# Kernel tuning notes

Hardware: AMD Instinct MI355X
Metric: run time of the kernel (lower is better)

Reference implementation:

```python
import jax, jax.numpy as jnp
import numpy as np

B, D, H, NSTEPS = 4096, 512, 2048, 16


def setup_inputs() -> dict:
    key = jax.random.key(0)
    k1, k2, k3, k4 = jax.random.split(key, 4)
    s_x = 1.0 / np.sqrt(D)
    s_h = 1.0 / np.sqrt(H)
    return {
        "z_in": jax.random.normal(k1, (B, D), dtype=jnp.float32),
        "Wx": jax.random.normal(k2, (D, H), dtype=jnp.float32) * s_x,
        "Wh": jax.random.normal(k3, (H, H), dtype=jnp.float32) * s_h,
        "bh": jnp.zeros((H,), dtype=jnp.float32),
        "Wout": jax.random.normal(k4, (H, D), dtype=jnp.float32) * s_h,
        "bout": jnp.zeros((D,), dtype=jnp.float32),
        "n_steps": NSTEPS,
    }


def reference(z_in, Wx, Wh, bh, Wout, bout, n_steps):
    # Input projection is identical every step (same z_in fed each iteration).
    xproj = z_in @ Wx + bh  # [B, H]
    h0 = jnp.zeros((z_in.shape[0], Wh.shape[0]), dtype=z_in.dtype)

    def step(h, _):
        h_new = jnp.tanh(xproj + h @ Wh)          # Elman RNN cell, hidden retained
        out = h_new @ Wout + bout                  # MLP head hidden -> latent
        return h_new, out

    _, outs = jax.lax.scan(step, h0, None, length=n_steps)  # [n_steps, B, D]
    return jnp.transpose(outs, (1, 0, 2))  # torch.stack(outs, 1) -> [B, n_steps, D]
```

## Files before the change

### kernel.cpp

```cpp
#include <hip/hip_runtime.h>
#include <hip/hip_bf16.h>
#include <stdint.h>

#define B_ 4096
#define D_ 512
#define H_ 2048
#define NS_ 16

typedef __bf16 bf16x8 __attribute__((ext_vector_type(8)));
typedef float f32x4 __attribute__((ext_vector_type(4)));
typedef short short4v __attribute__((ext_vector_type(4)));

__device__ __forceinline__ short f2bf(float f) {
  union { float f; uint32_t u; } c; c.f = f;
  uint32_t u = c.u;
  return (short)((u + 0x7fffu + ((u >> 16) & 1u)) >> 16);
}

__device__ __forceinline__ float tanh_fast(float x) {
  float e = __expf(2.0f * x);
  return 1.0f - 2.0f / (e + 1.0f);
}

__device__ __forceinline__ void gload16(const void* g, void* l) {
  __builtin_amdgcn_global_load_lds((const __attribute__((address_space(1))) void*)g,
                                   (__attribute__((address_space(3))) void*)l,
                                   16, 0, 0);
}

template<int BM, int BN, int EPI>
__global__ __launch_bounds__(256, 2) void gemm_bt(
    const short* __restrict__ A, const short* __restrict__ Bt, int K,
    const float* __restrict__ xproj, const float* __restrict__ bias,
    float* __restrict__ outf, short* __restrict__ outh, int ldN, int tout)
{
  constexpr int WM = BM / 2, WN = BN / 2;
  constexpr int RM = WM / 16, RN = WN / 16;
  __shared__ short lds[2][(BM + BN) * 32];
  const int tid = threadIdx.x, lane = tid & 63, wid = tid >> 6;
  const int wm = wid >> 1, wn = wid & 1;
  const int row0 = blockIdx.y * BM, col0 = blockIdx.x * BN;
  const short* Ag = A + (size_t)row0 * K;
  const short* Bg = Bt + (size_t)col0 * K;

  f32x4 acc[RM][RN];
#pragma unroll
  for (int m = 0; m < RM; ++m)
#pragma unroll
    for (int n = 0; n < RN; ++n)
      acc[m][n] = (f32x4){0.f, 0.f, 0.f, 0.f};

  const int nt = K >> 5;

  auto stage = [&](int kt, int buf) {
    const short* ga = Ag + (kt << 5);
#pragma unroll
    for (int i = 0; i < BM * 4; i += 256) {
      int slot = i + tid;
      gload16(ga + (size_t)(slot >> 2) * K + ((slot & 3) << 3), &lds[buf][slot * 8]);
    }
    const short* gb = Bg + (kt << 5);
#pragma unroll
    for (int i = 0; i < BN * 4; i += 256) {
      int slot = i + tid;
      gload16(gb + (size_t)(slot >> 2) * K + ((slot & 3) << 3),
              &lds[buf][BM * 32 + slot * 8]);
    }
  };

  stage(0, 0);
  __syncthreads();
  int cur = 0;
  const int kq = (lane >> 4) << 3;
  const int rr = lane & 15;
  for (int kt = 0; kt < nt; ++kt) {
    if (kt + 1 < nt) stage(kt + 1, cur ^ 1);
    const short* la = &lds[cur][(wm * WM) * 32];
    const short* lb = &lds[cur][BM * 32 + (wn * WN) * 32];
    bf16x8 a[RM], b[RN];
#pragma unroll
    for (int m = 0; m < RM; ++m)
      a[m] = *(const bf16x8*)(la + (m * 16 + rr) * 32 + kq);
#pragma unroll
    for (int n = 0; n < RN; ++n)
      b[n] = *(const bf16x8*)(lb + (n * 16 + rr) * 32 + kq);
#pragma unroll
    for (int m = 0; m < RM; ++m)
#pragma unroll
      for (int n = 0; n < RN; ++n)
        acc[m][n] = __builtin_amdgcn_mfma_f32_16x16x32_bf16(a[m], b[n], acc[m][n], 0, 0, 0);
    __syncthreads();
    cur ^= 1;
  }

  const int rb = row0 + wm * WM + ((lane >> 4) << 2);
  const int cb = col0 + wn * WN + (lane & 15);
#pragma unroll
  for (int m = 0; m < RM; ++m) {
#pragma unroll
    for (int n = 0; n < RN; ++n) {
      const int col = cb + n * 16;
#pragma unroll
      for (int r = 0; r < 4; ++r) {
        const int row = rb + m * 16 + r;
        float v = acc[m][n][r];
        if (EPI == 0) {
          outf[(size_t)row * ldN + col] = v + bias[col];
        } else if (EPI == 2) {
          outf[(size_t)row * (NS_ * D_) + tout * D_ + col] = v + bias[col];
        } else {
          if (col < H_) {
            float x = xproj[(size_t)row * H_ + col];
            outh[(size_t)row * H_ + col] = f2bf(tanh_fast(x + v));
          } else {
            int oc = col - H_;
            outf[(size_t)row * (NS_ * D_) + tout * D_ + oc] = v + bias[oc];
          }
        }
      }
    }
  }
}

__global__ void transpose_cvt(const float* __restrict__ in, short* __restrict__ out,
                              int R, int C) {
  __shared__ float tile[32][33];
  const int tx = threadIdx.x & 31, ty = threadIdx.x >> 5;
  const int c0 = blockIdx.x * 32, r0 = blockIdx.y * 32;
#pragma unroll
  for (int i = 0; i < 32; i += 8)
    tile[ty + i][tx] = in[(size_t)(r0 + ty + i) * C + c0 + tx];
  __syncthreads();
#pragma unroll
  for (int i = 0; i < 32; i += 8)
    out[(size_t)(c0 + ty + i) * R + r0 + tx] = f2bf(tile[tx][ty + i]);
}

__global__ void cvt_bf16_k(const float4* __restrict__ in, short4v* __restrict__ out, int n4) {
  int i = blockIdx.x * 256 + threadIdx.x;
  if (i >= n4) return;
  float4 v = in[i];
  short4v o;
  o[0] = f2bf(v.x); o[1] = f2bf(v.y); o[2] = f2bf(v.z); o[3] = f2bf(v.w);
  out[i] = o;
}

__global__ void tanh_h0_k(const float4* __restrict__ xp, short4v* __restrict__ h, int n4) {
  int i = blockIdx.x * 256 + threadIdx.x;
  if (i >= n4) return;
  float4 v = xp[i];
  short4v o;
  o[0] = f2bf(tanh_fast(v.x)); o[1] = f2bf(tanh_fast(v.y));
  o[2] = f2bf(tanh_fast(v.z)); o[3] = f2bf(tanh_fast(v.w));
  h[i] = o;
}

extern "C" void kernel_launch(void* const* d_in, const int* in_sizes, int n_in,
                              void* d_out, int out_size, void* d_ws, size_t ws_size,
                              hipStream_t stream) {
  const float* z    = (const float*)d_in[0];
  const float* Wx   = (const float*)d_in[1];
  const float* Wh   = (const float*)d_in[2];
  const float* bh   = (const float*)d_in[3];
  const float* Wout = (const float*)d_in[4];
  const float* bout = (const float*)d_in[5];
  float* out = (float*)d_out;

  short* zb    = (short*)d_ws;
  short* WxT   = zb + (size_t)B_ * D_;
  short* WcatT = WxT + (size_t)H_ * D_;
  short* WoutT = WcatT + (size_t)H_ * H_;
  short* h0    = WcatT + (size_t)(H_ + D_) * H_;
  short* h1    = h0 + (size_t)B_ * H_;
  float* xproj = (float*)(h1 + (size_t)B_ * H_);

  cvt_bf16_k<<<(B_ * D_ / 4 + 255) / 256, 256, 0, stream>>>((const float4*)z, (short4v*)zb, B_ * D_ / 4);
  transpose_cvt<<<dim3(H_ / 32, D_ / 32), 256, 0, stream>>>(Wx, WxT, D_, H_);
  transpose_cvt<<<dim3(H_ / 32, H_ / 32), 256, 0, stream>>>(Wh, WcatT, H_, H_);
  transpose_cvt<<<dim3(D_ / 32, H_ / 32), 256, 0, stream>>>(Wout, WoutT, H_, D_);

  gemm_bt<128, 128, 0><<<dim3(H_ / 128, B_ / 128), 256, 0, stream>>>(
      zb, WxT, D_, nullptr, bh, xproj, nullptr, H_, 0);
  tanh_h0_k<<<(B_ * H_ / 4 + 255) / 256, 256, 0, stream>>>((const float4*)xproj, (short4v*)h0, B_ * H_ / 4);

  short* hb[2] = {h0, h1};
  for (int t = 1; t <= 15; ++t) {
    const short* hp = hb[(t - 1) & 1];
    short* hn = hb[t & 1];
    gemm_bt<128, 128, 1><<<dim3((H_ + D_) / 128, B_ / 128), 256, 0, stream>>>(
        hp, WcatT, H_, xproj, bout, out, hn, 0, t - 1);
  }
  gemm_bt<128, 64, 2><<<dim3(D_ / 64, B_ / 128), 256, 0, stream>>>(
      hb[1], WoutT, H_, nullptr, bout, out, nullptr, 0, 15);
}
```

Measured before the change: 1.176 ms.

## Replace recurrent step GEMM with 256x256 tiled, 4-stage pipelined fused kernel

Adds a new kernel for the 15 recurrent steps. It uses 256x256 output tiles with 8 waves, a 4-deep LDS ring buffer fed by direct global-to-LDS loads, and an XOR-swizzled LDS layout to avoid bank conflicts. Explicit vmcnt waits, setprio and sched barriers interleave loads with MFMA, and block indices are remapped in a chiplet-aware way. The goal is higher arithmetic intensity and better latency hiding than the 128x128 double-buffered kernel, at the cost of a 128KB LDS footprint, heavy register pressure and only 160 workgroups.

After: 1.424 ms. +21.1%, slower.

```diff
diff --git a/kernel.cpp b/kernel.cpp
--- a/kernel.cpp
+++ b/kernel.cpp
@@ -26,6 +26,134 @@
   __builtin_amdgcn_global_load_lds((const __attribute__((address_space(1))) void*)g,
                                    (__attribute__((address_space(3))) void*)l,
                                    16, 0, 0);
+}
+
+__global__ __launch_bounds__(512, 2) void gemm256_fused(
+    const short* __restrict__ A, const short* __restrict__ Bt, int K,
+    const float* __restrict__ xproj, const float* __restrict__ bias,
+    float* __restrict__ outf, short* __restrict__ outh, int tout, int gridN)
+{
+  __shared__ short lds[65536];
+  char* const lbase = (char*)lds;
+  const int tid = threadIdx.x, lane = tid & 63, wid = tid >> 6;
+  const int wm = wid >> 2, wn = wid & 3;
+
+  const int nwg = gridDim.x;
+  const int cpx = nwg >> 3;
+  const int swz = ((int)blockIdx.x & 7) * cpx + ((int)blockIdx.x >> 3);
+  const int tm = swz / gridN, tn = swz % gridN;
+  const int row0 = tm * 256, col0 = tn * 256;
+
+  const int NT = K >> 5;
+
+  const int rA0 = wid * 32 + (lane >> 2);
+  const int rA1 = rA0 + 16;
+  const int sl = lane & 3;
+  const short* gA0 = A  + (size_t)(row0 + rA0) * K + ((sl ^ ((rA0 >> 1) & 3)) << 3);
+  const short* gA1 = A  + (size_t)(row0 + rA1) * K + ((sl ^ ((rA1 >> 1) & 3)) << 3);
+  const short* gB0 = Bt + (size_t)(col0 + rA0) * K + ((sl ^ ((rA0 >> 1) & 3)) << 3);
+  const short* gB1 = Bt + (size_t)(col0 + rA1) * K + ((sl ^ ((rA1 >> 1) & 3)) << 3);
+
+  const int rr = lane & 15, s = lane >> 4;
+  int offA[8], offB[4];
+#pragma unroll
+  for (int m = 0; m < 8; ++m) {
+    int r = wm * 128 + m * 16 + rr;
+    offA[m] = r * 64 + ((s ^ ((r >> 1) & 3)) << 4);
+  }
+#pragma unroll
+  for (int n = 0; n < 4; ++n) {
+    int r = wn * 64 + n * 16 + rr;
+    offB[n] = 16384 + r * 64 + ((s ^ ((r >> 1) & 3)) << 4);
+  }
+
+  f32x4 acc[8][4];
+#pragma unroll
+  for (int m = 0; m < 8; ++m)
+#pragma unroll
+    for (int n = 0; n < 4; ++n)
+      acc[m][n] = (f32x4){0.f, 0.f, 0.f, 0.f};
+
+  auto stageA = [&](int kt) {
+    char* da = lbase + (kt & 3) * 32768 + wid * 2048;
+    gload16(gA0 + (size_t)kt * 32, da);
+    gload16(gA1 + (size_t)kt * 32, da + 1024);
+  };
+  auto stageB = [&](int kt) {
+    char* db = lbase + (kt & 3) * 32768 + 16384 + wid * 2048;
+    gload16(gB0 + (size_t)kt * 32, db);
+    gload16(gB1 + (size_t)kt * 32, db + 1024);
+  };
+
+  stageA(0); stageB(0);
+  stageA(1); stageB(1);
+  stageA(2); stageB(2);
+
+  auto tile = [&](int kt, bool issue) {
+    __builtin_amdgcn_sched_barrier(0);
+    __builtin_amdgcn_s_barrier();
+    __builtin_amdgcn_sched_barrier(0);
+    const char* lb = lbase + (kt & 3) * 32768;
+    if (issue) stageA(kt + 3);
+    bf16x8 a[4], b[4];
+#pragma unroll
+    for (int m = 0; m < 4; ++m) a[m] = *(const bf16x8*)(lb + offA[m]);
+#pragma unroll
+    for (int n = 0; n < 4; ++n) b[n] = *(const bf16x8*)(lb + offB[n]);
+    __builtin_amdgcn_s_setprio(1);
+#pragma unroll
+    for (int m = 0; m < 4; ++m)
+#pragma unroll
+      for (int n = 0; n < 4; ++n)
+        acc[m][n] = __builtin_amdgcn_mfma_f32_16x16x32_bf16(a[m], b[n], acc[m][n], 0, 0, 0);
+    __builtin_amdgcn_s_setprio(0);
+    __builtin_amdgcn_sched_barrier(0);
+    if (issue) stageB(kt + 3);
+#pragma unroll
+    for (int m = 0; m < 4; ++m) a[m] = *(const bf16x8*)(lb + offA[4 + m]);
+    __builtin_amdgcn_s_setprio(1);
+#pragma unroll
+    for (int m = 0; m < 4; ++m)
+#pragma unroll
+      for (int n = 0; n < 4; ++n)
+        acc[4 + m][n] = __builtin_amdgcn_mfma_f32_16x16x32_bf16(a[m], b[n], acc[4 + m][n], 0, 0, 0);
+    __builtin_amdgcn_s_setprio(0);
+    __builtin_amdgcn_sched_barrier(0);
+  };
+
+  int kt = 0;
+  for (; kt < NT - 3; ++kt) {
+    asm volatile("s_waitcnt vmcnt(8)" ::: "memory");
+    tile(kt, true);
+  }
+  asm volatile("s_waitcnt vmcnt(8)" ::: "memory");
+  tile(NT - 3, false);
+  asm volatile("s_waitcnt vmcnt(4)" ::: "memory");
+  tile(NT - 2, false);
+  asm volatile("s_waitcnt vmcnt(0)" ::: "memory");
+  tile(NT - 1, false);
+
+  const int rb = row0 + wm * 128 + ((lane >> 4) << 2);
+  const int cb = col0 + wn * 64 + (lane & 15);
+#pragma unroll
+  for (int m = 0; m < 8; ++m) {
+#pragma unroll
+    for (int n = 0; n < 4; ++n) {
+      const int col = cb + n * 16;
+#pragma unroll
+      for (int r = 0; r < 4; ++r) {
+        const int row = rb + m * 16 + r;
+        float v = acc[m][n][r];
+        if (col < H_) {
+          float x = xproj[(size_t)row * H_ + col];
+          outh[(size_t)row * H_ + col] = f2bf(tanh_fast(x + v));
+        } else {
+          int oc = col - H_;
+          outf[(size_t)row * (NS_ * D_) + tout * D_ + oc] = v + bias[oc];
+        }
+      }
+    }
+  }
 }
 
 template<int BM, int BN, int EPI>
@@ -106,16 +234,8 @@
         float v = acc[m][n][r];
         if (EPI == 0) {
           outf[(size_t)row * ldN + col] = v + bias[col];
-        } else if (EPI == 2) {
+        } else {
           outf[(size_t)row * (NS_ * D_) + tout * D_ + col] = v + bias[col];
-        } else {
-          if (col < H_) {
-            float x = xproj[(size_t)row * H_ + col];
-            outh[(size_t)row * H_ + col] = f2bf(tanh_fast(x + v));
-          } else {
-            int oc = col - H_;
-            outf[(size_t)row * (NS_ * D_) + tout * D_ + oc] = v + bias[oc];
-          }
         }
       }
     }
@@ -187,8 +307,8 @@
   for (int t = 1; t <= 15; ++t) {
     const short* hp = hb[(t - 1) & 1];
     short* hn = hb[t & 1];
-    gemm_bt<128, 128, 1><<<dim3((H_ + D_) / 128, B_ / 128), 256, 0, stream>>>(
-        hp, WcatT, H_, xproj, bout, out, hn, 0, t - 1);
+    gemm256_fused<<<160, 512, 0, stream>>>(
+        hp, WcatT, H_, xproj, bout, out, hn, t - 1, 10);
   }
   gemm_bt<128, 64, 2><<<dim3(D_ / 64, B_ / 128), 256, 0, stream>>>(
       hb[1], WoutT, H_, nullptr, bout, out, nullptr, 0, 15);
```
